# Performance work log

Measured on AMD Instinct MI355X. Metric: run time of the kernel, lower is better.

The kernel has to match this reference:

```python
import jax, jax.numpy as jnp
import numpy as np
from jax import lax

N, T, D, H = 32, 1024, 512, 512


def setup_inputs() -> dict:
    key = jax.random.key(0)
    k1, k2, k3, k4 = jax.random.split(key, 4)
    x = jax.random.normal(k1, (N, T, D), dtype=jnp.float32)
    h0 = jax.random.normal(k2, (N, H), dtype=jnp.float32)
    Wx = jax.random.normal(k3, (D, 4 * H), dtype=jnp.float32) / np.sqrt(D)
    Wh = jax.random.normal(k4, (H, 4 * H), dtype=jnp.float32) / np.sqrt(H)
    b = jnp.zeros((4 * H,), dtype=jnp.float32)
    return {"x": x, "h0": h0, "Wx": Wx, "Wh": Wh, "b": b}


def reference(x, h0, Wx, Wh, b):
    # Precompute input-to-hidden projection for all timesteps (batched GEMM).
    # Mathematically identical to per-step x_t @ Wx in the original.
    xW = jnp.einsum('ntd,dk->ntk', x, Wx) + b  # (N, T, 4H)
    xW = jnp.swapaxes(xW, 0, 1)                # (T, N, 4H) for scan
    c0 = jnp.zeros_like(h0)

    def step(carry, xw_t):
        h, c = carry
        a = xw_t + h @ Wh                      # (N, 4H)
        a_i, a_f, a_o, a_g = jnp.split(a, 4, axis=1)
        i = jax.nn.sigmoid(a_i)
        f = jax.nn.sigmoid(a_f)
        o = jax.nn.sigmoid(a_o)
        g = jnp.tanh(a_g)
        c_next = f * c + i * g
        h_next = o * jnp.tanh(c_next)
        return (h_next, c_next), h_next

    _, hs = lax.scan(step, (h0, c0), xW)       # hs: (T, N, H)
    return jnp.swapaxes(hs, 0, 1)              # (N, T, H)
```

## Files before the change

kernel.cpp:

```cpp
#include <hip/hip_runtime.h>
#include <cstdint>

typedef _Float16 f16;
typedef f16      f16x8 __attribute__((ext_vector_type(8)));
typedef float    f32x4 __attribute__((ext_vector_type(4)));
typedef uint32_t u32;
typedef u32      u32x4 __attribute__((ext_vector_type(4)));

#define NB    32
#define TT    1024
#define DD    512
#define HH    512
#define NBHH  (NB*HH)
#define NWG   64

__device__ __forceinline__ float fsig(float x) {
    return __builtin_amdgcn_rcpf(1.0f + __expf(-x));
}
__device__ __forceinline__ float ftanh(float x) {
    return 1.0f - 2.0f * __builtin_amdgcn_rcpf(__expf(2.0f * x) + 1.0f);
}


__global__ void k_cast_x(const float* __restrict__ x, f16* __restrict__ x16) {
    int i = (blockIdx.x * 256 + threadIdx.x) * 8;
    float4 a = *(const float4*)(x + i);
    float4 c = *(const float4*)(x + i + 4);
    f16x8 v;
    v[0] = (f16)a.x; v[1] = (f16)a.y; v[2] = (f16)a.z; v[3] = (f16)a.w;
    v[4] = (f16)c.x; v[5] = (f16)c.y; v[6] = (f16)c.z; v[7] = (f16)c.w;
    *(f16x8*)(x16 + i) = v;
}

__global__ void k_perm_w(const float* __restrict__ W, f16* __restrict__ Wp) {
    int tid = blockIdx.x * 256 + threadIdx.x;
    int colp = tid >> 9, k = tid & 511;
    int wg = colp >> 5, c = colp & 31;
    int gate = c & 3, j = c >> 2;
    int col = gate * 512 + wg * 8 + j;
    Wp[tid] = (f16)W[k * 2048 + col];
}

__global__ void k_h0(const float* __restrict__ h0, f16* __restrict__ hb) {
    int i = blockIdx.x * 256 + threadIdx.x;
    hb[i] = (f16)h0[i];
}


__global__ void __launch_bounds__(256, 1) k_lstm(
    const f16* __restrict__ x16, const f16* __restrict__ Wxp,
    const f16* __restrict__ Whp, const float* __restrict__ bb,
    f16* hbuf, u32* flags, float* __restrict__ out)
{
    __shared__ unsigned char lds_h[32768];
    __shared__ u32           lds_pub[256];
    __shared__ float         lds_out[8192];

    const int wg  = blockIdx.x;
    const int tid = threadIdx.x;
    const int w   = tid >> 6;
    const int l   = tid & 63;
    const int mt  = w >> 1, nt = w & 1;
    const int lq  = l >> 4, lc = l & 15;

    const int colp = wg * 32 + nt * 16 + lc;
    const int gate = lc & 3, j_in = lc >> 2;
    const int hcol = wg * 8 + nt * 4 + j_in;
    const int hc8  = nt * 4 + j_in;
    const float bv = bb[gate * 512 + hcol];

    const int arow   = mt * 16 + lc;
    const int rm     = l & 3;
    const int n_mine = mt * 16 + lq * 4 + rm;

    f16x8 Bh[16], Bx[16];
    {
        const f16* ph = Whp + (size_t)colp * 512 + lq * 8;
        const f16* px = Wxp + (size_t)colp * 512 + lq * 8;
        #pragma unroll
        for (int ks = 0; ks < 16; ++ks) {
            Bh[ks] = *(const f16x8*)(ph + ks * 32);
            Bx[ks] = *(const f16x8*)(px + ks * 32);
        }
    }

    const f16* xptr = x16 + (size_t)arow * (TT * DD) + lq * 8;

    float c_reg[4] = {0.f, 0.f, 0.f, 0.f};

    for (int t = 0; t < TT; ++t) {
        f32x4 acc = {bv, bv, bv, bv};
        {
            const f16* xp = xptr + (size_t)t * DD;
            #pragma unroll
            for (int ks = 0; ks < 16; ++ks) {
                f16x8 ax = *(const f16x8*)(xp + ks * 32);
                acc = __builtin_amdgcn_mfma_f32_16x16x32_f16(ax, Bx[ks], acc, 0, 0, 0);
            }
        }
        if (t) {
            const u32* fl = flags + l;
            int guard = 0;
            for (;;) {
                u32 f;
                asm volatile("global_load_dword %0, %1, off sc0 sc1"
                             : "=v"(f) : "v"(fl));
                asm volatile("s_waitcnt vmcnt(0)" ::: "memory");
                if (__all(f >= (u32)t) || ++guard > (1 << 20)) break;
            }
        }
        __builtin_amdgcn_sched_barrier(0);
        {
            const char* gp = (const char*)(hbuf + ((t & 1) ? 0 : NBHH)) + tid * 16;
            u32x4 hv4[8];
            #pragma unroll
            for (int r = 0; r < 8; ++r) {
                const char* p = gp + r * 4096;
                asm volatile("global_load_dwordx4 %0, %1, off sc0 sc1"
                             : "=v"(hv4[r]) : "v"(p));
            }
            asm volatile("s_waitcnt vmcnt(0)" ::: "memory");
            __builtin_amdgcn_sched_barrier(0);
            const int inrow = (tid & 63) * 16;
            #pragma unroll
            for (int r = 0; r < 8; ++r) {
                int row = (tid >> 6) + 4 * r;
                int off = row * 1024 + (inrow ^ ((row & 7) << 4));
                *(u32x4*)&lds_h[off] = hv4[r];
            }
        }
        __syncthreads();
        {
            const int swz   = (arow & 7) << 4;
            const int baseA = arow * 1024;
            #pragma unroll
            for (int ks = 0; ks < 16; ++ks) {
                int inrowA = lq * 16 + ks * 64;
                u32x4 a = *(const u32x4*)&lds_h[baseA + (inrowA ^ swz)];
                acc = __builtin_amdgcn_mfma_f32_16x16x32_f16(
                          __builtin_bit_cast(f16x8, a), Bh[ks], acc, 0, 0, 0);
            }
        }
        float hv = 0.f;
        #pragma unroll
        for (int r = 0; r < 4; ++r) {
            float av = acc[r];
            int base = l & ~3;
            float ai = __shfl(av, base | 0, 64);
            float af = __shfl(av, base | 1, 64);
            float ao = __shfl(av, base | 2, 64);
            float ag = __shfl(av, base | 3, 64);
            float ig = fsig(ai), fg = fsig(af), og = fsig(ao), gg = ftanh(ag);
            float cn = fg * c_reg[r] + ig * gg;
            c_reg[r] = cn;
            float h = og * ftanh(cn);
            if (r == rm) hv = h;
        }
        {
            f16 h16 = (f16)hv;
            lds_pub[n_mine * 8 + hc8] = (u32)__builtin_bit_cast(unsigned short, h16);
            lds_out[(t & 31) * 256 + n_mine * 8 + hc8] = hv;
        }
        __syncthreads();
        if (w == 0) {
            if (tid < 32) {
                const u32* pp = lds_pub + tid * 8;
                u32 p0 = (pp[0] & 0xffffu) | (pp[1] << 16);
                u32 p1 = (pp[2] & 0xffffu) | (pp[3] << 16);
                u32 p2 = (pp[4] & 0xffffu) | (pp[5] << 16);
                u32 p3 = (pp[6] & 0xffffu) | (pp[7] << 16);
                u32x4 pv = {p0, p1, p2, p3};
                f16* hdst = hbuf + ((t & 1) ? NBHH : 0) + tid * HH + wg * 8;
                asm volatile("global_store_dwordx4 %0, %1, off sc0 sc1"
                             :: "v"(hdst), "v"(pv) : "memory");
            }
            asm volatile("s_waitcnt vmcnt(0)" ::: "memory");
            if (tid == 0) {
                u32 fv = (u32)(t + 1);
                u32* mf = flags + wg;
                asm volatile("global_store_dword %0, %1, off sc0 sc1"
                             :: "v"(mf), "v"(fv) : "memory");
            }
        }
        if ((t & 31) == 31) {
            #pragma unroll
            for (int r2 = 0; r2 < 8; ++r2) {
                int tau = tid + 256 * r2;
                int s   = tau >> 6;
                int n2  = (tau >> 1) & 31;
                int hc4 = tau & 1;
                float4 v = *(const float4*)&lds_out[s * 256 + n2 * 8 + hc4 * 4];
                float* op = out + (size_t)n2 * (TT * HH)
                                + (size_t)(t - 31 + s) * HH + wg * 8 + hc4 * 4;
                *(float4*)op = v;
            }
        }
    }
}


extern "C" void kernel_launch(void* const* d_in, const int* in_sizes, int n_in,
                              void* d_out, int out_size, void* d_ws, size_t ws_size,
                              hipStream_t stream)
{
    (void)in_sizes; (void)n_in; (void)out_size; (void)ws_size;
    const float* x  = (const float*)d_in[0];
    const float* h0 = (const float*)d_in[1];
    const float* Wx = (const float*)d_in[2];
    const float* Wh = (const float*)d_in[3];
    const float* b  = (const float*)d_in[4];
    float* out = (float*)d_out;

    char* ws = (char*)d_ws;
    u32* flags = (u32*)ws;
    f16* x16   = (f16*)(ws + (4 << 10));
    f16* Wxp   = (f16*)(ws + (4 << 10) + (32 << 20));
    f16* Whp   = (f16*)(ws + (4 << 10) + (34 << 20));
    f16* hbuf  = (f16*)(ws + (4 << 10) + (36 << 20));

    hipMemsetAsync(flags, 0, 4096, stream);
    k_cast_x<<<8192, 256, 0, stream>>>(x, x16);
    k_perm_w<<<4096, 256, 0, stream>>>(Wx, Wxp);
    k_perm_w<<<4096, 256, 0, stream>>>(Wh, Whp);
    k_h0<<<64, 256, 0, stream>>>(h0, hbuf + NBHH);
    k_lstm<<<NWG, 256, 0, stream>>>(x16, Wxp, Whp, b, hbuf, flags, out);
}
```

Measured before the change: 4.534 ms.

## Halve LSTM workgroup count to 32 with 512-thread blocks and single-wave flag polling

Repartitions the persistent recurrent kernel from 64 workgroups of 4 waves to 32 workgroups of 8 waves, each owning 16 hidden units. The aim is to shrink the per-step cross-workgroup barrier: there are half as many flags to publish and poll, and only wave 0 spins on them (with s_sleep) before a block-level barrier releases the rest. The output staging buffer now flushes every 8 timesteps instead of every 32. In exchange, two waves now share each SIMD and every step pays an extra __syncthreads, which may lengthen the latency-bound critical path.

```diff
diff --git a/kernel.cpp b/kernel.cpp
--- a/kernel.cpp
+++ b/kernel.cpp
@@ -12,7 +12,7 @@
 #define DD    512
 #define HH    512
 #define NBHH  (NB*HH)
-#define NWG   64
+#define NWG   32
 
 __device__ __forceinline__ float fsig(float x) {
     return __builtin_amdgcn_rcpf(1.0f + __expf(-x));
@@ -47,26 +47,27 @@
 }
 
 
-__global__ void __launch_bounds__(256, 1) k_lstm(
+__global__ void __launch_bounds__(512, 2) k_lstm(
     const f16* __restrict__ x16, const f16* __restrict__ Wxp,
     const f16* __restrict__ Whp, const float* __restrict__ bb,
     f16* hbuf, u32* flags, float* __restrict__ out)
 {
     __shared__ unsigned char lds_h[32768];
-    __shared__ u32           lds_pub[256];
-    __shared__ float         lds_out[8192];
+    __shared__ u32           lds_pub[512];
+    __shared__ float         lds_out[4096];
 
     const int wg  = blockIdx.x;
     const int tid = threadIdx.x;
     const int w   = tid >> 6;
     const int l   = tid & 63;
-    const int mt  = w >> 1, nt = w & 1;
+    const int ct  = w >> 1;
+    const int mt  = w & 1;
     const int lq  = l >> 4, lc = l & 15;
 
-    const int colp = wg * 32 + nt * 16 + lc;
+    const int colp = wg * 64 + ct * 16 + lc;
     const int gate = lc & 3, j_in = lc >> 2;
-    const int hcol = wg * 8 + nt * 4 + j_in;
-    const int hc8  = nt * 4 + j_in;
+    const int hc16 = (ct >> 1) * 8 + (ct & 1) * 4 + j_in;
+    const int hcol = wg * 16 + hc16;
     const float bv = bb[gate * 512 + hcol];
 
     const int arow   = mt * 16 + lc;
@@ -99,23 +100,27 @@
             }
         }
         if (t) {
-            const u32* fl = flags + l;
-            int guard = 0;
-            for (;;) {
-                u32 f;
-                asm volatile("global_load_dword %0, %1, off sc0 sc1"
-                             : "=v"(f) : "v"(fl));
-                asm volatile("s_waitcnt vmcnt(0)" ::: "memory");
-                if (__all(f >= (u32)t) || ++guard > (1 << 20)) break;
-            }
+            if (w == 0) {
+                const u32* fl = flags + (l & 31);
+                int guard = 0;
+                for (;;) {
+                    u32 f;
+                    asm volatile("global_load_dword %0, %1, off sc0 sc1"
+                                 : "=v"(f) : "v"(fl));
+                    asm volatile("s_waitcnt vmcnt(0)" ::: "memory");
+                    if (__all(f >= (u32)t) || ++guard > (1 << 20)) break;
+                    __builtin_amdgcn_s_sleep(1);
+                }
+            }
+            __syncthreads();
         }
         __builtin_amdgcn_sched_barrier(0);
         {
             const char* gp = (const char*)(hbuf + ((t & 1) ? 0 : NBHH)) + tid * 16;
-            u32x4 hv4[8];
-            #pragma unroll
-            for (int r = 0; r < 8; ++r) {
-                const char* p = gp + r * 4096;
+            u32x4 hv4[4];
+            #pragma unroll
+            for (int r = 0; r < 4; ++r) {
+                const char* p = gp + r * 8192;
                 asm volatile("global_load_dwordx4 %0, %1, off sc0 sc1"
                              : "=v"(hv4[r]) : "v"(p));
             }
@@ -123,8 +128,8 @@
             __builtin_amdgcn_sched_barrier(0);
             const int inrow = (tid & 63) * 16;
             #pragma unroll
-            for (int r = 0; r < 8; ++r) {
-                int row = (tid >> 6) + 4 * r;
+            for (int r = 0; r < 4; ++r) {
+                int row = (tid >> 6) + 8 * r;
                 int off = row * 1024 + (inrow ^ ((row & 7) << 4));
                 *(u32x4*)&lds_h[off] = hv4[r];
             }
@@ -158,40 +163,43 @@
         }
         {
             f16 h16 = (f16)hv;
-            lds_pub[n_mine * 8 + hc8] = (u32)__builtin_bit_cast(unsigned short, h16);
-            lds_out[(t & 31) * 256 + n_mine * 8 + hc8] = hv;
+            lds_pub[n_mine * 16 + hc16] = (u32)__builtin_bit_cast(unsigned short, h16);
+            lds_out[(t & 7) * 512 + n_mine * 16 + hc16] = hv;
         }
         __syncthreads();
         if (w == 0) {
-            if (tid < 32) {
-                const u32* pp = lds_pub + tid * 8;
+            {
+                const int row = l >> 1, half = l & 1;
+                const u32* pp = lds_pub + row * 16 + half * 8;
                 u32 p0 = (pp[0] & 0xffffu) | (pp[1] << 16);
                 u32 p1 = (pp[2] & 0xffffu) | (pp[3] << 16);
                 u32 p2 = (pp[4] & 0xffffu) | (pp[5] << 16);
                 u32 p3 = (pp[6] & 0xffffu) | (pp[7] << 16);
                 u32x4 pv = {p0, p1, p2, p3};
-                f16* hdst = hbuf + ((t & 1) ? NBHH : 0) + tid * HH + wg * 8;
+                f16* hdst = hbuf + ((t & 1) ? NBHH : 0)
+                          + row * HH + wg * 16 + half * 8;
                 asm volatile("global_store_dwordx4 %0, %1, off sc0 sc1"
                              :: "v"(hdst), "v"(pv) : "memory");
             }
             asm volatile("s_waitcnt vmcnt(0)" ::: "memory");
-            if (tid == 0) {
+            if (l == 0) {
                 u32 fv = (u32)(t + 1);
                 u32* mf = flags + wg;
                 asm volatile("global_store_dword %0, %1, off sc0 sc1"
                              :: "v"(mf), "v"(fv) : "memory");
             }
         }
-        if ((t & 31) == 31) {
-            #pragma unroll
-            for (int r2 = 0; r2 < 8; ++r2) {
-                int tau = tid + 256 * r2;
-                int s   = tau >> 6;
-                int n2  = (tau >> 1) & 31;
-                int hc4 = tau & 1;
-                float4 v = *(const float4*)&lds_out[s * 256 + n2 * 8 + hc4 * 4];
-                float* op = out + (size_t)n2 * (TT * HH)
-                                + (size_t)(t - 31 + s) * HH + wg * 8 + hc4 * 4;
+        if ((t & 7) == 7) {
+            #pragma unroll
+            for (int k2 = 0; k2 < 2; ++k2) {
+                int tau = tid + 512 * k2;
+                int s   = tau >> 7;
+                int rem = tau & 127;
+                int row = rem >> 2;
+                int cq  = rem & 3;
+                float4 v = *(const float4*)&lds_out[s * 512 + row * 16 + cq * 4];
+                float* op = out + (size_t)row * (TT * HH)
+                                + (size_t)(t - 7 + s) * HH + wg * 16 + cq * 4;
                 *(float4*)op = v;
             }
         }
@@ -223,5 +231,5 @@
     k_perm_w<<<4096, 256, 0, stream>>>(Wx, Wxp);
     k_perm_w<<<4096, 256, 0, stream>>>(Wh, Whp);
     k_h0<<<64, 256, 0, stream>>>(h0, hbuf + NBHH);
-    k_lstm<<<NWG, 256, 0, stream>>>(x16, Wxp, Whp, b, hbuf, flags, out);
-}
+    k_lstm<<<NWG, 512, 0, stream>>>(x16, Wxp, Whp, b, hbuf, flags, out);
+}
```

New measurement: 6.268 ms. 1.38x slower.
